# Optimization experiments

Hardware: AMD Instinct MI355X
Metric: run time of the kernel (lower is better)

The kernel has to match this reference:

```python
import jax, jax.numpy as jnp
import numpy as np

N_CLS = 3

def _conv(x, w, b):
    # 3x3 'same' conv, NHWC / HWIO
    return jax.lax.conv_general_dilated(
        x, w, window_strides=(1, 1), padding='SAME',
        dimension_numbers=('NHWC', 'HWIO', 'NHWC')) + b


def setup_inputs() -> dict:
    key = jax.random.key(0)
    ks = jax.random.split(key, 24)
    B, H, W, C0 = 4, 512, 512, 32   # decoder outputs['0']
    C4 = 256                         # encoder features['4'] channels
    f32 = jnp.float32
    p = lambda k, s: jax.random.normal(k, s, f32) * 0.05
    inp = {
        'x0': jax.random.normal(ks[0], (B, H, W, C0), f32),
        'f4': jax.random.normal(ks[1], (B, 32, 32, C4), f32),
        # offset head: BatchConv2D(64) x2 (BN folded) + Conv2D(2*n_cls)
        'Wo1': p(ks[2], (3, 3, C0, 64)), 'bo1': jnp.zeros((64,), f32),
        'Wo2': p(ks[3], (3, 3, 64, 64)), 'bo2': jnp.zeros((64,), f32),
        'Wo3': p(ks[4], (3, 3, 64, 2 * N_CLS)), 'bo3': jnp.zeros((2 * N_CLS,), f32),
        # weight head: BatchConv2D(64) x2 + Conv2D(n_cls)
        'Ww1': p(ks[5], (3, 3, C0, 64)), 'bw1': jnp.zeros((64,), f32),
        'Ww2': p(ks[6], (3, 3, 64, 64)), 'bw2': jnp.zeros((64,), f32),
        'Ww3': p(ks[7], (3, 3, 64, N_CLS)), 'bw3': jnp.zeros((N_CLS,), f32),
        # classification head: GAP -> Dense(128) -> Dense(128) -> Dense(n_cls, softmax)
        'Wc1': p(ks[8], (C4, 128)), 'bc1': jnp.zeros((128,), f32),
        'Wc2': p(ks[9], (128, 128)), 'bc2': jnp.zeros((128,), f32),
        'Wc3': p(ks[10], (128, N_CLS)), 'bc3': jnp.zeros((N_CLS,), f32),
    }
    return inp


def reference(x0, f4, Wo1, bo1, Wo2, bo2, Wo3, bo3,
              Ww1, bw1, Ww2, bw2, Ww3, bw3,
              Wc1, bc1, Wc2, bc2, Wc3, bc3):
    # offset head -> [B,H,W,2*n_cls]
    h = jax.nn.relu(_conv(x0, Wo1, bo1))
    h = jax.nn.relu(_conv(h, Wo2, bo2))
    offsets_full = _conv(h, Wo3, bo3)
    # weight head -> [B,H,W,n_cls]
    g = jax.nn.relu(_conv(x0, Ww1, bw1))
    g = jax.nn.relu(_conv(g, Ww2, bw2))
    weights_full = _conv(g, Ww3, bw3)
    # classification head on features['4']
    gap = jnp.mean(f4, axis=(1, 2))                 # [B,C4]
    z = jax.nn.relu(gap @ Wc1 + bc1)
    z = jax.nn.relu(z @ Wc2 + bc2)
    pred_cls = jax.nn.softmax(z @ Wc3 + bc3, axis=-1)  # [B,n_cls]
    # inference path: cls = argmax(pred_cls)
    cls = jnp.argmax(pred_cls, axis=-1).astype(jnp.int32)  # [B]
    # tf.gather(offsets, stack([cls*2, cls*2+1],-1), axis=-1, batch_dims=1)
    idx2 = jnp.stack([cls * 2, cls * 2 + 1], axis=-1)[:, None, None, :]  # [B,1,1,2]
    offsets = jnp.take_along_axis(
        offsets_full, jnp.broadcast_to(idx2, offsets_full.shape[:3] + (2,)), axis=-1)
    # tf.gather(weights, cls[:,None], axis=-1, batch_dims=1)
    idx1 = cls[:, None, None, None]
    weights = jnp.take_along_axis(
        weights_full, jnp.broadcast_to(idx1, weights_full.shape[:3] + (1,)), axis=-1)
    return offsets, weights, pred_cls
```

## Files before the change

kernel.cpp:

```cpp
#include <hip/hip_runtime.h>
#include <hip/hip_bf16.h>
#include <math.h>

typedef __attribute__((ext_vector_type(8))) short short8;
typedef __attribute__((ext_vector_type(4))) short short4v;
typedef __attribute__((ext_vector_type(4))) float floatx4;
typedef unsigned short ushort_t;
typedef unsigned int uint_t;

__device__ __forceinline__ ushort_t f2bf(float x) {
    uint_t u = __float_as_uint(x);
    uint_t r = (u + 0x7fffu + ((u >> 16) & 1u)) >> 16;
    return (ushort_t)r;
}
__device__ __forceinline__ short4v pack4(float a, float b, float c, float d) {
    union { __hip_bfloat162 h; uint_t u; } lo, hi;
    lo.h = __float22bfloat162_rn(make_float2(a, b));
    hi.h = __float22bfloat162_rn(make_float2(c, d));
    short4v r;
    r[0] = (short)(lo.u & 0xffffu); r[1] = (short)(lo.u >> 16);
    r[2] = (short)(hi.u & 0xffffu); r[3] = (short)(hi.u >> 16);
    return r;
}
__device__ __forceinline__ short8 pack8(float4 v0, float4 v1) {
    short4v lo = pack4(v0.x, v0.y, v0.z, v0.w);
    short4v hi = pack4(v1.x, v1.y, v1.z, v1.w);
    short8 pk;
    pk[0] = lo[0]; pk[1] = lo[1]; pk[2] = lo[2]; pk[3] = lo[3];
    pk[4] = hi[0]; pk[5] = hi[1]; pk[6] = hi[2]; pk[7] = hi[3];
    return pk;
}

__global__ void prep_all(const float* __restrict__ W1a, const float* __restrict__ W2a,
                         const float* __restrict__ W1b, const float* __restrict__ W2b,
                         const float* __restrict__ W3a, const float* __restrict__ W3b,
                         ushort_t* __restrict__ wt, ushort_t* __restrict__ w3t,
                         const float* __restrict__ f4, float* __restrict__ part) {
    __shared__ float4 red[256];
    int bi = blockIdx.x, t = threadIdx.x;
    if (bi < 432) {
        int i = bi * 256 + t;
        const float* W; int off; int C;
        if (i < 18432)      { W = W1a; off = i;         C = 32; }
        else if (i < 55296) { W = W2a; off = i - 18432; C = 64; }
        else if (i < 73728) { W = W1b; off = i - 55296; C = 32; }
        else                { W = W2b; off = i - 73728; C = 64; }
        int pt = C * 64;
        int tap = off / pt, rem = off - tap * pt;
        int k4 = rem >> 9, rem2 = rem & 511;
        int co = rem2 >> 3, j = rem2 & 7;
        int ci = k4 * 8 + j;
        wt[i] = f2bf(W[(size_t)(tap * C + ci) * 64 + co]);
    } else if (bi < 648) {
        int i = (bi - 432) * 256 + t;
        int branch = i / 27648; int r = i - branch * 27648;
        int cls = r / 9216; int r2 = r - cls * 9216;
        int t2 = r2 >> 9; int r3 = r2 & 511;
        int qq = r3 >> 7; int r4 = r3 & 127;
        int ch = r4 >> 3; int j = r4 & 7;
        int tap = t2 >> 1, kh = t2 & 1;
        int ci = kh * 32 + qq * 8 + j;
        int NCH = branch ? 1 : 2, C3 = branch ? 3 : 6;
        const float* W3 = branch ? W3b : W3a;
        ushort_t v = 0;
        if (ch < NCH) v = f2bf(W3[(size_t)(tap * 64 + ci) * C3 + cls * NCH + ch]);
        w3t[i] = v;
    } else {
        int g = bi - 648;
        int c = g & 7, b = g >> 3;
        int ci4 = t & 63, po = t >> 6;
        const float* f = f4 + ((size_t)b * 1024 + c * 128) * 256;
        float4 s = {0, 0, 0, 0};
        for (int i = 0; i < 32; ++i) {
            float4 v = *(const float4*)&f[(size_t)(i * 4 + po) * 256 + ci4 * 4];
            s.x += v.x; s.y += v.y; s.z += v.z; s.w += v.w;
        }
        red[t] = s;
        __syncthreads();
        if (t < 64) {
            float4 a = red[t], b2 = red[64 + t], c2 = red[128 + t], d2 = red[192 + t];
            float4 gg;
            gg.x = a.x + b2.x + c2.x + d2.x;
            gg.y = a.y + b2.y + c2.y + d2.y;
            gg.z = a.z + b2.z + c2.z + d2.z;
            gg.w = a.w + b2.w + c2.w + d2.w;
            *(float4*)&part[((b * 8 + c) << 8) + t * 4] = gg;
        }
    }
}

__global__ void cls_finish(const float* __restrict__ part,
                           const float* __restrict__ Wc1, const float* __restrict__ bc1,
                           const float* __restrict__ Wc2, const float* __restrict__ bc2,
                           const float* __restrict__ Wc3, const float* __restrict__ bc3,
                           float* __restrict__ pred_out, int* __restrict__ cls_out) {
    int b = blockIdx.x;
    int t = threadIdx.x;
    __shared__ float gap[256];
    __shared__ float z1[128];
    __shared__ float z2[128];
    __shared__ float lg[3];
    float s = 0.f;
    for (int c = 0; c < 8; ++c) s += part[((b * 8 + c) << 8) + t];
    gap[t] = s * (1.0f / 1024.0f);
    __syncthreads();
    if (t < 128) {
        float a = bc1[t];
        for (int i = 0; i < 256; ++i) a += gap[i] * Wc1[i * 128 + t];
        z1[t] = fmaxf(a, 0.f);
    }
    __syncthreads();
    if (t < 128) {
        float a = bc2[t];
        for (int i = 0; i < 128; ++i) a += z1[i] * Wc2[i * 128 + t];
        z2[t] = fmaxf(a, 0.f);
    }
    __syncthreads();
    if (t < 3) {
        float a = bc3[t];
        for (int i = 0; i < 128; ++i) a += z2[i] * Wc3[i * 3 + t];
        lg[t] = a;
    }
    __syncthreads();
    if (t == 0) {
        float m = fmaxf(lg[0], fmaxf(lg[1], lg[2]));
        float e0 = expf(lg[0] - m), e1 = expf(lg[1] - m), e2 = expf(lg[2] - m);
        float ssum = e0 + e1 + e2;
        pred_out[b * 3 + 0] = e0 / ssum;
        pred_out[b * 3 + 1] = e1 / ssum;
        pred_out[b * 3 + 2] = e2 / ssum;
        int idx = 0; float best = lg[0];
        if (lg[1] > best) { best = lg[1]; idx = 1; }
        if (lg[2] > best) { best = lg[2]; idx = 2; }
        cls_out[b] = idx;
    }
}

#define X0_E 0
#define X0_KS 2600
#define H1_E 10400
#define H1_KS 2056
#define H2_E 0
#define H2_LD 76
#define SF_F 7448
#define LDS_E 26848

__global__ __launch_bounds__(256, 3)
void fused_branch(const float* __restrict__ x0,
                  const ushort_t* __restrict__ W1o_t, const ushort_t* __restrict__ W2o_t,
                  const ushort_t* __restrict__ W1w_t, const ushort_t* __restrict__ W2w_t,
                  const ushort_t* __restrict__ w3t,
                  const float* __restrict__ bo1, const float* __restrict__ bo2,
                  const float* __restrict__ bw1, const float* __restrict__ bw2,
                  const float* __restrict__ bo3, const float* __restrict__ bw3,
                  const int* __restrict__ clsp,
                  float* __restrict__ off_out, float* __restrict__ w_out) {
    __shared__ __align__(16) ushort_t lds[LDS_E];
    float* ldsf = (float*)lds;
    const int t = threadIdx.x;
    const int b = blockIdx.y;
    const int z = blockIdx.z;
    const ushort_t* W1t = z ? W1w_t : W1o_t;
    const ushort_t* W2t = z ? W2w_t : W2o_t;
    const ushort_t* W3T = w3t + z * 27648;
    const float* B1 = z ? bw1 : bo1;
    const float* B2 = z ? bw2 : bo2;
    const float* B3 = z ? bw3 : bo3;
    float* outp = z ? w_out : off_out;
    const int NCH = z ? 1 : 2;

    const int tileY = blockIdx.x / 43, tileX = blockIdx.x - tileY * 43;
    const int ty0 = tileY * 12, tx0 = tileX * 12;
    const bool edge = (tileY == 0) | (tileY == 42) | (tileX == 0) | (tileX == 42);
    const int lane = t & 63, wave = t >> 6;
    const int m = lane & 15, q = lane >> 4;
    const int cls = clsp[b];

    if (!edge) {
        for (int idx = t; idx < 1296; idx += 256) {
            int pix = idx >> 2, qq = idx & 3;
            int py = pix / 18, px = pix - py * 18;
            const float* xp = x0 + (((size_t)b * 512 + (ty0 - 3 + py)) * 512 + (tx0 - 3 + px)) * 32 + qq * 8;
            *(short8*)&lds[X0_E + qq * X0_KS + pix * 8] =
                pack8(*(const float4*)xp, *(const float4*)(xp + 4));
        }
    } else {
        for (int idx = t; idx < 1296; idx += 256) {
            int pix = idx >> 2, qq = idx & 3;
            int py = pix / 18, px = pix - py * 18;
            int gy = ty0 - 3 + py, gx = tx0 - 3 + px;
            float4 v0 = {0, 0, 0, 0}, v1 = {0, 0, 0, 0};
            if ((uint_t)gy < 512u && (uint_t)gx < 512u) {
                const float* xp = x0 + (((size_t)b * 512 + gy) * 512 + gx) * 32 + qq * 8;
                v0 = *(const float4*)xp;
                v1 = *(const float4*)(xp + 4);
            }
            *(short8*)&lds[X0_E + qq * X0_KS + pix * 8] = pack8(v0, v1);
        }
    }
    __syncthreads();

    {
        floatx4 acc[4][4];
#pragma unroll
        for (int mi = 0; mi < 4; ++mi) {
            float4 bb = *(const float4*)&B1[mi * 16 + q * 4];
            floatx4 ib = (floatx4){bb.x, bb.y, bb.z, bb.w};
#pragma unroll
            for (int n = 0; n < 4; ++n) acc[mi][n] = ib;
        }
        const int wsel = q * 512 + m * 8;
        short8 Anow[4];
#pragma unroll
        for (int mi = 0; mi < 4; ++mi)
            Anow[mi] = *(const short8*)&W1t[wsel + mi * 128];

        for (int tap = 0; tap < 9; ++tap) {
            int tn = tap < 8 ? tap + 1 : 8;
            short8 Anext[4];
#pragma unroll
            for (int mi = 0; mi < 4; ++mi)
                Anext[mi] = *(const short8*)&W1t[tn * 2048 + wsel + mi * 128];
            int dy = tap / 3, dx = tap - dy * 3;
            short8 Bx[4];
#pragma unroll
            for (int n = 0; n < 4; ++n) {
                int ptile = n * 4 + wave;
                Bx[n] = *(const short8*)&lds[X0_E + q * X0_KS + ((ptile + dy) * 18 + (m + dx)) * 8];
            }
#pragma unroll
            for (int mi = 0; mi < 4; ++mi)
#pragma unroll
                for (int n = 0; n < 4; ++n)
                    acc[mi][n] = __builtin_amdgcn_mfma_f32_16x16x32_bf16(Anow[mi], Bx[n], acc[mi][n], 0, 0, 0);
#pragma unroll
            for (int mi = 0; mi < 4; ++mi) Anow[mi] = Anext[mi];
        }
        if (!edge) {
#pragma unroll
            for (int mi = 0; mi < 4; ++mi) {
                int ks = mi * 2 + (q >> 1), lo = (q & 1) * 4;
#pragma unroll
                for (int n = 0; n < 4; ++n) {
                    int ptile = n * 4 + wave;
                    floatx4 a = acc[mi][n];
                    *(short4v*)&lds[H1_E + ks * H1_KS + (ptile * 16 + m) * 8 + lo] =
                        pack4(fmaxf(a[0], 0.f), fmaxf(a[1], 0.f), fmaxf(a[2], 0.f), fmaxf(a[3], 0.f));
                }
            }
        } else {
#pragma unroll
            for (int mi = 0; mi < 4; ++mi) {
                int ks = mi * 2 + (q >> 1), lo = (q & 1) * 4;
#pragma unroll
                for (int n = 0; n < 4; ++n) {
                    int ptile = n * 4 + wave;
                    int gy = ty0 - 2 + ptile, gx = tx0 - 2 + m;
                    bool ok = ((uint_t)gy < 512u) && ((uint_t)gx < 512u);
                    floatx4 a = acc[mi][n];
                    float v0 = ok ? fmaxf(a[0], 0.f) : 0.f;
                    float v1 = ok ? fmaxf(a[1], 0.f) : 0.f;
                    float v2 = ok ? fmaxf(a[2], 0.f) : 0.f;
                    float v3 = ok ? fmaxf(a[3], 0.f) : 0.f;
                    *(short4v*)&lds[H1_E + ks * H1_KS + (ptile * 16 + m) * 8 + lo] = pack4(v0, v1, v2, v3);
                }
            }
        }
    }
    __syncthreads();

    {
        floatx4 acc[4][4];
#pragma unroll
        for (int mi = 0; mi < 4; ++mi) {
            float4 bb = *(const float4*)&B2[mi * 16 + q * 4];
            floatx4 ib = (floatx4){bb.x, bb.y, bb.z, bb.w};
#pragma unroll
            for (int n = 0; n < 4; ++n) acc[mi][n] = ib;
        }
        int hb2[4];
#pragma unroll
        for (int n = 0; n < 4; ++n) {
            int p0 = (n * 4 + wave) * 16 + m;
            int pv = p0 < 196 ? p0 : 195;
            int py = pv / 14, px = pv - py * 14;
            hb2[n] = py * 16 + px;
        }
        const int wsel = q * 512 + m * 8;
        short8 Anow[4];
#pragma unroll
        for (int mi = 0; mi < 4; ++mi)
            Anow[mi] = *(const short8*)&W2t[wsel + mi * 128];

        for (int s = 0; s < 18; ++s) {
            int tap = s >> 1, kh = s & 1;
            int sn = s < 17 ? s + 1 : 17;
            short8 Anext[4];
#pragma unroll
            for (int mi = 0; mi < 4; ++mi)
                Anext[mi] = *(const short8*)&W2t[(sn >> 1) * 4096 + ((sn & 1) * 4) * 512 + wsel + mi * 128];
            int dy = tap / 3, dx = tap - dy * 3;
            short8 Bx[4];
#pragma unroll
            for (int n = 0; n < 4; ++n)
                Bx[n] = *(const short8*)&lds[H1_E + (kh * 4 + q) * H1_KS + (hb2[n] + dy * 16 + dx) * 8];
#pragma unroll
            for (int mi = 0; mi < 4; ++mi)
#pragma unroll
                for (int n = 0; n < 4; ++n) {
                    int ptile = n * 4 + wave;
                    if (ptile < 13)
                        acc[mi][n] = __builtin_amdgcn_mfma_f32_16x16x32_bf16(Anow[mi], Bx[n], acc[mi][n], 0, 0, 0);
                }
#pragma unroll
            for (int mi = 0; mi < 4; ++mi) Anow[mi] = Anext[mi];
        }
        __syncthreads();
#pragma unroll
        for (int n = 0; n < 4; ++n) {
            int ptile = n * 4 + wave;
            if (ptile >= 13) continue;
            int p = ptile * 16 + m;
            bool pok = p < 196;
            bool ok = pok;
            if (edge) {
                int py = p / 14, px = p - py * 14;
                int gy = ty0 - 1 + py, gx = tx0 - 1 + px;
                ok = pok && ((uint_t)gy < 512u) && ((uint_t)gx < 512u);
            }
#pragma unroll
            for (int mi = 0; mi < 4; ++mi) {
                floatx4 a = acc[mi][n];
                float v0 = ok ? fmaxf(a[0], 0.f) : 0.f;
                float v1 = ok ? fmaxf(a[1], 0.f) : 0.f;
                float v2 = ok ? fmaxf(a[2], 0.f) : 0.f;
                float v3 = ok ? fmaxf(a[3], 0.f) : 0.f;
                if (pok)
                    *(short4v*)&lds[H2_E + p * H2_LD + mi * 16 + q * 4] = pack4(v0, v1, v2, v3);
            }
        }
    }
    __syncthreads();

    {
        floatx4 acc3[9];
#pragma unroll
        for (int n = 0; n < 9; ++n) acc3[n] = (floatx4){0.f, 0.f, 0.f, 0.f};
        int hb3[9];
#pragma unroll
        for (int n = 0; n < 9; ++n) {
            int p = n * 16 + m;
            int py = p / 12, px = p - py * 12;
            hb3[n] = py * 14 + px;
        }
        const ushort_t* W3c = W3T + cls * 9216;
        for (int t2 = wave; t2 < 18; t2 += 4) {
            int tap = t2 >> 1, kh = t2 & 1;
            int dy = tap / 3, dx = tap - dy * 3;
            short8 Aw = *(const short8*)&W3c[t2 * 512 + q * 128 + m * 8];
#pragma unroll
            for (int n = 0; n < 9; ++n) {
                short8 Bh = *(const short8*)&lds[H2_E + (hb3[n] + dy * 14 + dx) * H2_LD + kh * 32 + q * 8];
                acc3[n] = __builtin_amdgcn_mfma_f32_16x16x32_bf16(Aw, Bh, acc3[n], 0, 0, 0);
            }
        }
        float* sf = ldsf + SF_F;
        if (q == 0) {
#pragma unroll
            for (int n = 0; n < 9; ++n) {
                float2 v = {acc3[n][0], acc3[n][1]};
                *(float2*)&sf[wave * 288 + n * 32 + m * 2] = v;
            }
        }
    }
    __syncthreads();
    if (t < 144) {
        float* sf = ldsf + SF_F;
        int p = t;
        int base = (p >> 4) * 32 + (p & 15) * 2;
        float a0 = sf[base] + sf[288 + base] + sf[576 + base] + sf[864 + base];
        int py = p / 12, px = p - py * 12;
        int gy = ty0 + py, gx = tx0 + px;
        if (gy < 512 && gx < 512) {
            size_t ob = (((size_t)b * 512 + gy) * 512 + gx) * NCH;
            outp[ob] = a0 + B3[cls * NCH + 0];
            if (NCH == 2) {
                float a1 = sf[base + 1] + sf[288 + base + 1] + sf[576 + base + 1] + sf[864 + base + 1];
                outp[ob + 1] = a1 + B3[cls * NCH + 1];
            }
        }
    }
}

extern "C" void kernel_launch(void* const* d_in, const int* in_sizes, int n_in,
                              void* d_out, int out_size, void* d_ws, size_t ws_size,
                              hipStream_t stream) {
    const float* x0  = (const float*)d_in[0];
    const float* f4  = (const float*)d_in[1];
    const float* Wo1 = (const float*)d_in[2];  const float* bo1 = (const float*)d_in[3];
    const float* Wo2 = (const float*)d_in[4];  const float* bo2 = (const float*)d_in[5];
    const float* Wo3 = (const float*)d_in[6];  const float* bo3 = (const float*)d_in[7];
    const float* Ww1 = (const float*)d_in[8];  const float* bw1 = (const float*)d_in[9];
    const float* Ww2 = (const float*)d_in[10]; const float* bw2 = (const float*)d_in[11];
    const float* Ww3 = (const float*)d_in[12]; const float* bw3 = (const float*)d_in[13];
    const float* Wc1 = (const float*)d_in[14]; const float* bc1 = (const float*)d_in[15];
    const float* Wc2 = (const float*)d_in[16]; const float* bc2 = (const float*)d_in[17];
    const float* Wc3 = (const float*)d_in[18]; const float* bc3 = (const float*)d_in[19];

    float* out = (float*)d_out;
    float* offsets_out = out;
    float* weights_out = out + 2097152;
    float* pred_out    = out + 3145728;

    int* cls_ws = (int*)d_ws;
    ushort_t* wt  = (ushort_t*)((char*)d_ws + 16);
    ushort_t* w3t = (ushort_t*)((char*)d_ws + 221200);
    float* gap_part = (float*)((char*)d_ws + 331792);

    const ushort_t* W1o_t = wt;
    const ushort_t* W2o_t = wt + 18432;
    const ushort_t* W1w_t = wt + 55296;
    const ushort_t* W2w_t = wt + 73728;

    prep_all<<<680, 256, 0, stream>>>(Wo1, Wo2, Ww1, Ww2, Wo3, Ww3, wt, w3t, f4, gap_part);
    cls_finish<<<4, 256, 0, stream>>>(gap_part, Wc1, bc1, Wc2, bc2, Wc3, bc3, pred_out, cls_ws);

    dim3 grid(43 * 43, 4, 2);
    fused_branch<<<grid, 256, 0, stream>>>(x0,
                                           W1o_t, W2o_t, W1w_t, W2w_t, w3t,
                                           bo1, bo2, bw1, bw2,
                                           bo3, bw3,
                                           cls_ws, offsets_out, weights_out);
}
```

Measured before the change: 606.3 us.

## Load conv1 input directly from global memory, dropping the LDS staging buffer

The first conv layer now reads x0 straight from global memory per tap and converts it to bf16 in registers, instead of first staging an 18x18 halo tile in LDS behind a barrier. This shrinks the LDS footprint (the x0 region is removed and the H2 stride is reduced) and drops one sync. It also removes the ptile<13 guard in the conv2 MFMA loop so every tile runs unconditionally. In exchange, each x0 element is re-read from global/L2 up to nine times across taps and converted each time, adding memory traffic and VALU work.

```diff
diff --git a/kernel.cpp b/kernel.cpp
--- a/kernel.cpp
+++ b/kernel.cpp
@@ -136,14 +136,12 @@
     }
 }
 
-#define X0_E 0
-#define X0_KS 2600
-#define H1_E 10400
+#define H1_E 0
 #define H1_KS 2056
 #define H2_E 0
-#define H2_LD 76
-#define SF_F 7448
-#define LDS_E 26848
+#define H2_LD 72
+#define SF_F 7056
+#define LDS_E 16448
 
 __global__ __launch_bounds__(256, 3)
 void fused_branch(const float* __restrict__ x0,
@@ -176,30 +174,6 @@
     const int m = lane & 15, q = lane >> 4;
     const int cls = clsp[b];
 
-    if (!edge) {
-        for (int idx = t; idx < 1296; idx += 256) {
-            int pix = idx >> 2, qq = idx & 3;
-            int py = pix / 18, px = pix - py * 18;
-            const float* xp = x0 + (((size_t)b * 512 + (ty0 - 3 + py)) * 512 + (tx0 - 3 + px)) * 32 + qq * 8;
-            *(short8*)&lds[X0_E + qq * X0_KS + pix * 8] =
-                pack8(*(const float4*)xp, *(const float4*)(xp + 4));
-        }
-    } else {
-        for (int idx = t; idx < 1296; idx += 256) {
-            int pix = idx >> 2, qq = idx & 3;
-            int py = pix / 18, px = pix - py * 18;
-            int gy = ty0 - 3 + py, gx = tx0 - 3 + px;
-            float4 v0 = {0, 0, 0, 0}, v1 = {0, 0, 0, 0};
-            if ((uint_t)gy < 512u && (uint_t)gx < 512u) {
-                const float* xp = x0 + (((size_t)b * 512 + gy) * 512 + gx) * 32 + qq * 8;
-                v0 = *(const float4*)xp;
-                v1 = *(const float4*)(xp + 4);
-            }
-            *(short8*)&lds[X0_E + qq * X0_KS + pix * 8] = pack8(v0, v1);
-        }
-    }
-    __syncthreads();
-
     {
         floatx4 acc[4][4];
 #pragma unroll
@@ -214,6 +188,7 @@
 #pragma unroll
         for (int mi = 0; mi < 4; ++mi)
             Anow[mi] = *(const short8*)&W1t[wsel + mi * 128];
+        const float* xrow = x0 + ((size_t)((b * 512 + ty0 - 3)) * 512 + (tx0 - 3 + m)) * 32 + q * 8;
 
         for (int tap = 0; tap < 9; ++tap) {
             int tn = tap < 8 ? tap + 1 : 8;
@@ -223,10 +198,26 @@
                 Anext[mi] = *(const short8*)&W1t[tn * 2048 + wsel + mi * 128];
             int dy = tap / 3, dx = tap - dy * 3;
             short8 Bx[4];
-#pragma unroll
-            for (int n = 0; n < 4; ++n) {
-                int ptile = n * 4 + wave;
-                Bx[n] = *(const short8*)&lds[X0_E + q * X0_KS + ((ptile + dy) * 18 + (m + dx)) * 8];
+            if (!edge) {
+#pragma unroll
+                for (int n = 0; n < 4; ++n) {
+                    int row = n * 4 + wave + dy;
+                    const float* xp = xrow + (size_t)(row * 512 + dx) * 32;
+                    Bx[n] = pack8(*(const float4*)xp, *(const float4*)(xp + 4));
+                }
+            } else {
+#pragma unroll
+                for (int n = 0; n < 4; ++n) {
+                    int gy = ty0 - 3 + n * 4 + wave + dy;
+                    int gx = tx0 - 3 + m + dx;
+                    float4 f0 = {0, 0, 0, 0}, f1 = {0, 0, 0, 0};
+                    if ((uint_t)gy < 512u && (uint_t)gx < 512u) {
+                        const float* xp = x0 + (((size_t)b * 512 + gy) * 512 + gx) * 32 + q * 8;
+                        f0 = *(const float4*)xp;
+                        f1 = *(const float4*)(xp + 4);
+                    }
+                    Bx[n] = pack8(f0, f1);
+                }
             }
 #pragma unroll
             for (int mi = 0; mi < 4; ++mi)
@@ -307,11 +298,8 @@
 #pragma unroll
             for (int mi = 0; mi < 4; ++mi)
 #pragma unroll
-                for (int n = 0; n < 4; ++n) {
-                    int ptile = n * 4 + wave;
-                    if (ptile < 13)
-                        acc[mi][n] = __builtin_amdgcn_mfma_f32_16x16x32_bf16(Anow[mi], Bx[n], acc[mi][n], 0, 0, 0);
-                }
+                for (int n = 0; n < 4; ++n)
+                    acc[mi][n] = __builtin_amdgcn_mfma_f32_16x16x32_bf16(Anow[mi], Bx[n], acc[mi][n], 0, 0, 0);
 #pragma unroll
             for (int mi = 0; mi < 4; ++mi) Anow[mi] = Anext[mi];
         }
```

After: 969.2 us. +59.8%, slower.
